# Optimization experiments

Measured on AMD Instinct MI355X. Metric: run time of the kernel, lower is better.

## Reference

```python
import jax, jax.numpy as jnp
import numpy as np

PAD = 32      # person_attrs_dim
NZ = 64       # num_zones
T = 32768     # number of timesteps
D = PAD + 1 + NZ  # 97, input dim to the MLP


def _ln(x, g, b, eps=1e-5):
    # LayerNorm over the last (only) axis of a 1-D vector
    m = jnp.mean(x)
    v = jnp.mean((x - m) ** 2)
    return g * (x - m) / jnp.sqrt(v + eps) + b


def setup_inputs() -> dict:
    key = jax.random.key(0)
    ks = jax.random.split(key, 24)

    def xav(k, shape):  # xavier_normal_ for nn.Linear weight [out, in]
        std = np.sqrt(2.0 / (shape[0] + shape[1])).astype(np.float32)
        return std * jax.random.normal(k, shape, dtype=jnp.float32)

    def lng(k, n):  # layernorm gain (perturbed from 1 so grads are non-trivial)
        return 1.0 + 0.1 * jax.random.normal(k, (n,), dtype=jnp.float32)

    def lnb(k, n):
        return 0.1 * jax.random.normal(k, (n,), dtype=jnp.float32)

    inp = {
        "person_attrs": jax.random.normal(ks[0], (PAD,), dtype=jnp.float32),
        "times": jax.random.uniform(ks[1], (T,), dtype=jnp.float32) * 24.0,
        "zone_features": jax.random.normal(ks[2], (NZ, 16), dtype=jnp.float32),
        "edge_index": jax.random.randint(ks[3], (2, 256), 0, NZ, dtype=jnp.int32),
        # input_norm
        "g0": lng(ks[4], D), "b0": lnb(ks[5], D),
        # encoder1: Linear(D,256) + LN(256)
        "W1": xav(ks[6], (256, D)), "b1": jnp.zeros((256,), jnp.float32),
        "g1": lng(ks[7], 256), "be1": lnb(ks[8], 256),
        # encoder2: Linear(256,128) + LN(128)
        "W2": xav(ks[9], (128, 256)), "b2": jnp.zeros((128,), jnp.float32),
        "g2": lng(ks[10], 128), "be2": lnb(ks[11], 128),
        # output_layer: Linear(128,64) + LN(64) + Linear(64,NZ)
        "W3": xav(ks[12], (64, 128)), "b3": jnp.zeros((64,), jnp.float32),
        "g3": lng(ks[13], 64), "be3": lnb(ks[14], 64),
        "W4": xav(ks[15], (NZ, 64)), "b4": jnp.zeros((NZ,), jnp.float32),
    }
    return inp


def reference(person_attrs, times, zone_features, edge_index,
              g0, b0, W1, b1, g1, be1, W2, b2, g2, be2,
              W3, b3, g3, be3, W4, b4):
    nz = W4.shape[0]
    # set_graph_data: symmetric adjacency with self-loops (zone_features unused)
    u, v = edge_index[0], edge_index[1]
    A = jnp.zeros((nz, nz), jnp.float32).at[u, v].set(1.0).at[v, u].set(1.0)
    A = jnp.maximum(A, jnp.eye(nz, dtype=jnp.float32))

    def step(zone, t):
        onehot = jax.nn.one_hot(zone, nz, dtype=jnp.float32)
        x = jnp.concatenate([person_attrs, t[None], onehot])  # [D]
        x = _ln(x, g0, b0)
        h = jax.nn.relu(_ln(W1 @ x + b1, g1, be1))   # dropout is eval-mode identity
        h = jax.nn.relu(_ln(W2 @ h + b2, g2, be2))
        h = jax.nn.relu(_ln(W3 @ h + b3, g3, be3))
        raw = W4 @ h + b4                            # [nz] raw logits
        row = A[zone]
        # (raw/temp with invalid=-50/temp) * temp  ==  where(valid, raw, -50)
        pred = jnp.where(row > 0, raw, jnp.float32(-50.0))
        nxt = jnp.argmax(jnp.where(row > 0, raw, -jnp.inf)).astype(zone.dtype)
        return nxt, pred

    _, zone_logits = jax.lax.scan(step, jnp.array(0, jnp.int32), times)
    return zone_logits  # [T, nz]
```

## Files before the change

kernel.cpp:

```cpp
#include <hip/hip_runtime.h>
#include <stdint.h>

typedef __attribute__((ext_vector_type(8))) short bf16x8;
typedef __attribute__((ext_vector_type(4))) float f32x4;
typedef __attribute__((ext_vector_type(4))) unsigned int u32x4;
typedef __attribute__((ext_vector_type(2))) unsigned int u32x2;

#define MFMA(a, b, c) __builtin_amdgcn_mfma_f32_16x16x32_bf16(a, b, c, 0, 0, 0)

__device__ __forceinline__ unsigned short f2b(float x) {
  unsigned u = __float_as_uint(x);
  return (unsigned short)((u + 0x7fffu + ((u >> 16) & 1u)) >> 16);
}
__device__ __forceinline__ float b2f(unsigned short h) {
  return __uint_as_float(((unsigned)h) << 16);
}

struct u2 { unsigned hi, lo; };
__device__ __forceinline__ u2 split2(float h0, float h1) {
  unsigned u0 = __float_as_uint(h0), u1 = __float_as_uint(h1);
  u2 r;
  r.hi = (u0 >> 16) | (u1 & 0xffff0000u);
  float r0 = h0 - __uint_as_float(u0 & 0xffff0000u);
  float r1 = h1 - __uint_as_float(u1 & 0xffff0000u);
  r.lo = (__float_as_uint(r0) >> 16) | (__float_as_uint(r1) & 0xffff0000u);
  return r;
}

#define SWZ(row, col) ((col) ^ ((((row) >> 2) & 1) << 4) ^ ((((row) >> 3) & 1) << 2))


__global__ void k_prep(const float* __restrict__ pa, const float* __restrict__ g0,
                       const float* __restrict__ b0, const float* __restrict__ W1,
                       const float* __restrict__ b1,
                       float* __restrict__ c_pa, float* __restrict__ w_t,
                       float* __restrict__ c_g, float* __restrict__ c_const,
                       float* __restrict__ scal, float* __restrict__ wzT,
                       float* __restrict__ wzZ) {
  int j = threadIdx.x;
  const float* wr = W1 + j * 97;
  float cg = 0.f, cc = 0.f, cp = 0.f;
  for (int k = 0; k < 97; ++k) { float w = wr[k]; cg += w * g0[k]; cc += w * b0[k]; }
  for (int k = 0; k < 32; ++k) cp += wr[k] * g0[k] * pa[k];
  c_g[j] = cg;
  c_const[j] = cc + b1[j];
  c_pa[j] = cp;
  w_t[j] = wr[32] * g0[32];
  for (int z = 0; z < 64; ++z) {
    float v = wr[33 + z] * g0[33 + z];
    wzT[j * 64 + z] = v;
    wzZ[z * 256 + j] = v;
  }
  if (j == 0) {
    float s = 0.f, q = 0.f;
    for (int k = 0; k < 32; ++k) { float x = pa[k]; s += x; q += x * x; }
    scal[0] = s; scal[1] = q;
  }
}

__global__ void k_prep2(const float* __restrict__ c_pa, const float* __restrict__ w_t,
                        const float* __restrict__ c_g, const float* __restrict__ c_const,
                        const float* __restrict__ wzT, float* __restrict__ st) {
  int tid = threadIdx.x;
  if (tid < 64) {
    int z = tid;
    float A = 0.f, Q = 0.f, dpa = 0.f, dwt = 0.f, dcg = 0.f, dcc = 0.f;
    for (int k = 0; k < 256; ++k) {
      float wz = wzT[k * 64 + z];
      A += wz; Q = fmaf(wz, wz, Q);
      dpa = fmaf(c_pa[k], wz, dpa);
      dwt = fmaf(w_t[k], wz, dwt);
      dcg = fmaf(c_g[k], wz, dcg);
      dcc = fmaf(c_const[k], wz, dcc);
    }
    st[z] = A; st[64 + z] = Q; st[128 + z] = dpa;
    st[192 + z] = dwt; st[256 + z] = dcg; st[320 + z] = dcc;
  } else {
    int lane = tid - 64;
    float acc[14];
    #pragma unroll
    for (int m = 0; m < 14; ++m) acc[m] = 0.f;
    for (int k = lane; k < 256; k += 64) {
      float P = c_pa[k], W = w_t[k], G = c_g[k], C = c_const[k];
      acc[0] += P; acc[1] += W; acc[2] += G; acc[3] += C;
      acc[4] = fmaf(P, P, acc[4]); acc[5] = fmaf(P, W, acc[5]);
      acc[6] = fmaf(P, G, acc[6]); acc[7] = fmaf(P, C, acc[7]);
      acc[8] = fmaf(W, W, acc[8]); acc[9] = fmaf(W, G, acc[9]);
      acc[10] = fmaf(W, C, acc[10]); acc[11] = fmaf(G, G, acc[11]);
      acc[12] = fmaf(G, C, acc[12]); acc[13] = fmaf(C, C, acc[13]);
    }
    #pragma unroll
    for (int off = 1; off < 64; off <<= 1) {
      #pragma unroll
      for (int m = 0; m < 14; ++m) acc[m] += __shfl_xor(acc[m], off, 64);
    }
    if (lane == 0) {
      #pragma unroll
      for (int m = 0; m < 14; ++m) st[386 + m] = acc[m];
    }
  }
}

__global__ void k_scal2st(const float* __restrict__ scal, float* __restrict__ st) {
  if (threadIdx.x < 2) st[384 + threadIdx.x] = scal[threadIdx.x];
}

__global__ void k_adj(const int* __restrict__ ei, unsigned long long* __restrict__ adj) {
  int t = threadIdx.x;
  if (t < 64) adj[t] = 1ull << t;
  __syncthreads();
  int u = ei[t] & 63, v = ei[256 + t] & 63;
  atomicOr(&adj[u], 1ull << v);
  atomicOr(&adj[v], 1ull << u);
}

__global__ void k_wsplit(const float* __restrict__ W2, const float* __restrict__ W3,
                         const float* __restrict__ W4,
                         unsigned short* __restrict__ W2Ah, unsigned short* __restrict__ W2Al,
                         unsigned short* __restrict__ W3Ah, unsigned short* __restrict__ W3Al,
                         unsigned short* __restrict__ W4Ah, unsigned short* __restrict__ W4Al) {
  int idx = blockIdx.x * 256 + threadIdx.x;
  float w; unsigned short* ph; unsigned short* pl; int o;
  if (idx < 32768) {
    int mt = idx >> 12, kt = (idx >> 9) & 7, lane = (idx >> 3) & 63, j = idx & 7;
    int m = mt * 16 + (lane & 15), k = kt * 32 + (lane >> 4) * 8 + j;
    w = W2[m * 256 + k]; ph = W2Ah; pl = W2Al; o = idx;
  } else if (idx < 40960) {
    int r = idx - 32768;
    int mt = r >> 11, kt = (r >> 9) & 3, lane = (r >> 3) & 63, j = r & 7;
    int m = mt * 16 + (lane & 15), k = kt * 32 + (lane >> 4) * 8 + j;
    w = W3[m * 128 + k]; ph = W3Ah; pl = W3Al; o = r;
  } else if (idx < 45056) {
    int r = idx - 40960;
    int mt = r >> 10, kt = (r >> 9) & 1, lane = (r >> 3) & 63, j = r & 7;
    int m = mt * 16 + (lane & 15), k = kt * 32 + (lane >> 4) * 8 + j;
    w = W4[m * 64 + k]; ph = W4Ah; pl = W4Al; o = r;
  } else return;
  unsigned short hb = f2b(w);
  ph[o] = hb;
  pl[o] = f2b(w - b2f(hb));
}


__global__ __launch_bounds__(256, 4) void k_pass1(
    const float* __restrict__ times,
    const float* __restrict__ c_pa, const float* __restrict__ w_t,
    const float* __restrict__ c_g, const float* __restrict__ c_const,
    const float* __restrict__ wzT, const float* __restrict__ st,
    const unsigned short* __restrict__ W2Ah, const unsigned short* __restrict__ W2Al,
    const unsigned short* __restrict__ W3Ah, const unsigned short* __restrict__ W3Al,
    const unsigned short* __restrict__ W4Ah, const unsigned short* __restrict__ W4Al,
    const float* __restrict__ b2, const float* __restrict__ b3,
    const float* __restrict__ b4,
    const float* __restrict__ g1, const float* __restrict__ be1,
    const float* __restrict__ g2, const float* __restrict__ be2,
    const float* __restrict__ g3, const float* __restrict__ be3,
    const unsigned long long* __restrict__ adj,
    unsigned char* __restrict__ nxt) {
  __shared__ __align__(16) char region[32768];
  __shared__ float u_lds[256];
  __shared__ float ps[512];

  unsigned short* B1hi = (unsigned short*)region;
  unsigned short* B1lo = (unsigned short*)(region + 16384);
  unsigned short* B2hi = (unsigned short*)region;
  unsigned short* B2lo = (unsigned short*)(region + 16384);
  unsigned short* B3hi = (unsigned short*)region;
  unsigned short* B3lo = (unsigned short*)(region + 8192);
  unsigned long long* pk = (unsigned long long*)ps;

  const int tid = threadIdx.x;
  const int lane = tid & 63;
  const int l15 = lane & 15;
  const int lhi = lane >> 4;
  const int w = __builtin_amdgcn_readfirstlane(tid >> 6);
  const int i = blockIdx.x;

  const float t = times[i];
  const float m0 = (st[384] + t + 1.0f) * (1.0f / 97.0f);
  const float e2 = (st[385] + t * t + 1.0f) * (1.0f / 97.0f);
  const float alpha = 1.0f / sqrtf(e2 - m0 * m0 + 1e-5f);
  const float gma = -m0 * alpha;

  const f32x4 zero4 = {0.f, 0.f, 0.f, 0.f};

  {
    int k = tid;
    float u = fmaf(t, w_t[k], c_pa[k]);
    u = fmaf(alpha, u, c_const[k]);
    u = fmaf(gma, c_g[k], u);
    u_lds[k] = u;
    float su = u, sq = u * u;
    #pragma unroll
    for (int off = 1; off < 64; off <<= 1) {
      su += __shfl_xor(su, off, 64);
      sq += __shfl_xor(sq, off, 64);
    }
    if (lane == 0) { ps[w] = su; ps[256 + w] = sq; }
  }
  __syncthreads();
  float mu1, inv1;
  {
    float U1 = ps[0] + ps[1] + ps[2] + ps[3];
    float Qu = ps[256] + ps[257] + ps[258] + ps[259];
    float A1 = st[lane], Qz = st[64 + lane];
    float dpa = st[128 + lane], dwt = st[192 + lane];
    float dcg = st[256 + lane], dcc = st[320 + lane];
    float s1 = fmaf(alpha, A1, U1);
    float uwz = fmaf(alpha, fmaf(t, dwt, dpa), fmaf(gma, dcg, dcc));
    float s2 = Qu + 2.0f * alpha * uwz + alpha * alpha * Qz;
    mu1 = s1 * (1.0f / 256.0f);
    inv1 = 1.0f / sqrtf(s2 * (1.0f / 256.0f) - mu1 * mu1 + 1e-5f);
  }

  f32x4 acc[2][4];
  #pragma unroll
  for (int a = 0; a < 2; ++a)
    #pragma unroll
    for (int b = 0; b < 4; ++b) acc[a][b] = zero4;

  u32x4 hh[4], hl[4];

  #pragma unroll
  for (int q = 0; q < 4; ++q) {
    int kb = w * 32 + q * 8;
    f32x4 u0 = *(const f32x4*)(u_lds + kb);
    f32x4 u1v = *(const f32x4*)(u_lds + kb + 4);
    float hbuf[8];
    #pragma unroll
    for (int j = 0; j < 8; ++j) {
      int k = kb + j;
      float u = (j < 4) ? u0[j] : u1v[j - 4];
      float p = fmaf(alpha, wzT[k * 64 + lane], u);
      float gi = g1[k] * inv1;
      float bb = fmaf(-mu1, gi, be1[k]);
      hbuf[j] = fmaxf(fmaf(p, gi, bb), 0.f);
    }
    #pragma unroll
    for (int e = 0; e < 4; ++e) {
      u2 s = split2(hbuf[2 * e], hbuf[2 * e + 1]);
      hh[q][e] = s.hi; hl[q][e] = s.lo;
    }
  }
  #pragma unroll
  for (int q = 0; q < 4; ++q) {
    int slotd = ((w * 4 + lhi) * 64 + q * 16 + l15) * 4;
    *(u32x4*)((unsigned*)B1hi + slotd) = hh[q];
    *(u32x4*)((unsigned*)B1lo + slotd) = hl[q];
  }
  __syncthreads();

  #pragma unroll
  for (int q = 0; q < 4; ++q) {
    int kb = 128 + w * 32 + q * 8;
    f32x4 u0 = *(const f32x4*)(u_lds + kb);
    f32x4 u1v = *(const f32x4*)(u_lds + kb + 4);
    float hbuf[8];
    #pragma unroll
    for (int j = 0; j < 8; ++j) {
      int k = kb + j;
      float u = (j < 4) ? u0[j] : u1v[j - 4];
      float p = fmaf(alpha, wzT[k * 64 + lane], u);
      float gi = g1[k] * inv1;
      float bb = fmaf(-mu1, gi, be1[k]);
      hbuf[j] = fmaxf(fmaf(p, gi, bb), 0.f);
    }
    #pragma unroll
    for (int e = 0; e < 4; ++e) {
      u2 s = split2(hbuf[2 * e], hbuf[2 * e + 1]);
      hh[q][e] = s.hi; hl[q][e] = s.lo;
    }
  }
  for (int kt = 0; kt < 4; ++kt) {
    bf16x8 a0h = *(const bf16x8*)(W2Ah + (((2 * w + 0) * 8 + kt) * 64 + lane) * 8);
    bf16x8 a0l = *(const bf16x8*)(W2Al + (((2 * w + 0) * 8 + kt) * 64 + lane) * 8);
    bf16x8 a1h = *(const bf16x8*)(W2Ah + (((2 * w + 1) * 8 + kt) * 64 + lane) * 8);
    bf16x8 a1l = *(const bf16x8*)(W2Al + (((2 * w + 1) * 8 + kt) * 64 + lane) * 8);
    #pragma unroll
    for (int nt = 0; nt < 4; ++nt) {
      bf16x8 bh = *(const bf16x8*)(B1hi + ((kt * 4 + nt) * 64 + lane) * 8);
      bf16x8 bl = *(const bf16x8*)(B1lo + ((kt * 4 + nt) * 64 + lane) * 8);
      acc[0][nt] = MFMA(a0h, bh, acc[0][nt]);
      acc[0][nt] = MFMA(a0h, bl, acc[0][nt]);
      acc[0][nt] = MFMA(a0l, bh, acc[0][nt]);
      acc[1][nt] = MFMA(a1h, bh, acc[1][nt]);
      acc[1][nt] = MFMA(a1h, bl, acc[1][nt]);
      acc[1][nt] = MFMA(a1l, bh, acc[1][nt]);
    }
  }
  __syncthreads();
  #pragma unroll
  for (int q = 0; q < 4; ++q) {
    int slotd = ((w * 4 + lhi) * 64 + q * 16 + l15) * 4;
    *(u32x4*)((unsigned*)B1hi + slotd) = hh[q];
    *(u32x4*)((unsigned*)B1lo + slotd) = hl[q];
  }
  __syncthreads();
  for (int kt = 0; kt < 4; ++kt) {
    int ktg = 4 + kt;
    bf16x8 a0h = *(const bf16x8*)(W2Ah + (((2 * w + 0) * 8 + ktg) * 64 + lane) * 8);
    bf16x8 a0l = *(const bf16x8*)(W2Al + (((2 * w + 0) * 8 + ktg) * 64 + lane) * 8);
    bf16x8 a1h = *(const bf16x8*)(W2Ah + (((2 * w + 1) * 8 + ktg) * 64 + lane) * 8);
    bf16x8 a1l = *(const bf16x8*)(W2Al + (((2 * w + 1) * 8 + ktg) * 64 + lane) * 8);
    #pragma unroll
    for (int nt = 0; nt < 4; ++nt) {
      bf16x8 bh = *(const bf16x8*)(B1hi + ((kt * 4 + nt) * 64 + lane) * 8);
      bf16x8 bl = *(const bf16x8*)(B1lo + ((kt * 4 + nt) * 64 + lane) * 8);
      acc[0][nt] = MFMA(a0h, bh, acc[0][nt]);
      acc[0][nt] = MFMA(a0h, bl, acc[0][nt]);
      acc[0][nt] = MFMA(a0l, bh, acc[0][nt]);
      acc[1][nt] = MFMA(a1h, bh, acc[1][nt]);
      acc[1][nt] = MFMA(a1h, bl, acc[1][nt]);
      acc[1][nt] = MFMA(a1l, bh, acc[1][nt]);
    }
  }

  #pragma unroll
  for (int mti = 0; mti < 2; ++mti) {
    f32x4 bv = *(const f32x4*)(b2 + w * 32 + mti * 16 + lhi * 4);
    #pragma unroll
    for (int nt = 0; nt < 4; ++nt) acc[mti][nt] += bv;
  }
  {
    #pragma unroll
    for (int nt = 0; nt < 4; ++nt) {
      float x1 = 0.f, x2 = 0.f;
      #pragma unroll
      for (int mti = 0; mti < 2; ++mti)
        #pragma unroll
        for (int r = 0; r < 4; ++r) { float v = acc[mti][nt][r]; x1 += v; x2 += v * v; }
      x1 += __shfl_xor(x1, 16, 64); x1 += __shfl_xor(x1, 32, 64);
      x2 += __shfl_xor(x2, 16, 64); x2 += __shfl_xor(x2, 32, 64);
      if (lane < 16) {
        ps[w * 64 + nt * 16 + lane] = x1;
        ps[256 + w * 64 + nt * 16 + lane] = x2;
      }
    }
  }
  __syncthreads();

  {
    float mu2v[4], iv2v[4];
    #pragma unroll
    for (int nt = 0; nt < 4; ++nt) {
      int c = nt * 16 + l15;
      float a = ps[c] + ps[64 + c] + ps[128 + c] + ps[192 + c];
      float b = ps[256 + c] + ps[320 + c] + ps[384 + c] + ps[448 + c];
      mu2v[nt] = a * (1.0f / 128.0f);
      iv2v[nt] = 1.0f / sqrtf(b * (1.0f / 128.0f) - mu2v[nt] * mu2v[nt] + 1e-5f);
    }
    f32x4 g2v[2], be2v[2];
    #pragma unroll
    for (int mti = 0; mti < 2; ++mti) {
      g2v[mti]  = *(const f32x4*)(g2  + w * 32 + mti * 16 + lhi * 4);
      be2v[mti] = *(const f32x4*)(be2 + w * 32 + mti * 16 + lhi * 4);
    }
    #pragma unroll
    for (int mti = 0; mti < 2; ++mti)
      #pragma unroll
      for (int nt = 0; nt < 4; ++nt) {
        float h[4];
        #pragma unroll
        for (int r = 0; r < 4; ++r) {
          float G = g2v[mti][r] * iv2v[nt];
          float B = fmaf(-mu2v[nt], G, be2v[mti][r]);
          h[r] = fmaxf(fmaf(acc[mti][nt][r], G, B), 0.f);
        }
        u2 s01 = split2(h[0], h[1]);
        u2 s23 = split2(h[2], h[3]);
        int base = ((w * 4 + nt) * 64 + (2 * mti + (lhi >> 1)) * 16 + l15) * 8
                 + 4 * (lhi & 1);
        u32x2 vh = {s01.hi, s23.hi};
        u32x2 vl = {s01.lo, s23.lo};
        *(u32x2*)(B2hi + base) = vh;
        *(u32x2*)(B2lo + base) = vl;
      }
  }
  __syncthreads();

  f32x4 acc2[4];
  #pragma unroll
  for (int b = 0; b < 4; ++b) acc2[b] = zero4;
  for (int kt = 0; kt < 4; ++kt) {
    bf16x8 ah = *(const bf16x8*)(W3Ah + ((w * 4 + kt) * 64 + lane) * 8);
    bf16x8 al = *(const bf16x8*)(W3Al + ((w * 4 + kt) * 64 + lane) * 8);
    #pragma unroll
    for (int nt = 0; nt < 4; ++nt) {
      bf16x8 bh = *(const bf16x8*)(B2hi + ((kt * 4 + nt) * 64 + lane) * 8);
      bf16x8 bl = *(const bf16x8*)(B2lo + ((kt * 4 + nt) * 64 + lane) * 8);
      acc2[nt] = MFMA(ah, bh, acc2[nt]);
      acc2[nt] = MFMA(ah, bl, acc2[nt]);
      acc2[nt] = MFMA(al, bh, acc2[nt]);
    }
  }
  {
    f32x4 bv = *(const f32x4*)(b3 + w * 16 + lhi * 4);
    #pragma unroll
    for (int nt = 0; nt < 4; ++nt) acc2[nt] += bv;
  }
  {
    #pragma unroll
    for (int nt = 0; nt < 4; ++nt) {
      float x1 = 0.f, x2 = 0.f;
      #pragma unroll
      for (int r = 0; r < 4; ++r) { float v = acc2[nt][r]; x1 += v; x2 += v * v; }
      x1 += __shfl_xor(x1, 16, 64); x1 += __shfl_xor(x1, 32, 64);
      x2 += __shfl_xor(x2, 16, 64); x2 += __shfl_xor(x2, 32, 64);
      if (lane < 16) {
        ps[w * 64 + nt * 16 + lane] = x1;
        ps[256 + w * 64 + nt * 16 + lane] = x2;
      }
    }
  }
  __syncthreads();

  {
    float mu3v[4], iv3v[4];
    #pragma unroll
    for (int nt = 0; nt < 4; ++nt) {
      int c = nt * 16 + l15;
      float a = ps[c] + ps[64 + c] + ps[128 + c] + ps[192 + c];
      float b = ps[256 + c] + ps[320 + c] + ps[384 + c] + ps[448 + c];
      mu3v[nt] = a * (1.0f / 64.0f);
      iv3v[nt] = 1.0f / sqrtf(b * (1.0f / 64.0f) - mu3v[nt] * mu3v[nt] + 1e-5f);
    }
    f32x4 g3v  = *(const f32x4*)(g3  + w * 16 + lhi * 4);
    f32x4 be3v = *(const f32x4*)(be3 + w * 16 + lhi * 4);
    #pragma unroll
    for (int nt = 0; nt < 4; ++nt) {
      float h[4];
      #pragma unroll
      for (int r = 0; r < 4; ++r) {
        float G = g3v[r] * iv3v[nt];
        float B = fmaf(-mu3v[nt], G, be3v[r]);
        h[r] = fmaxf(fmaf(acc2[nt][r], G, B), 0.f);
      }
      u2 s01 = split2(h[0], h[1]);
      u2 s23 = split2(h[2], h[3]);
      int base = (((w >> 1) * 4 + nt) * 64 + (2 * (w & 1) + (lhi >> 1)) * 16 + l15) * 8
               + 4 * (lhi & 1);
      u32x2 vh = {s01.hi, s23.hi};
      u32x2 vl = {s01.lo, s23.lo};
      *(u32x2*)(B3hi + base) = vh;
      *(u32x2*)(B3lo + base) = vl;
    }
  }
  __syncthreads();

  f32x4 acc3[4];
  #pragma unroll
  for (int b = 0; b < 4; ++b) acc3[b] = zero4;
  for (int kt = 0; kt < 2; ++kt) {
    bf16x8 ah = *(const bf16x8*)(W4Ah + ((w * 2 + kt) * 64 + lane) * 8);
    bf16x8 al = *(const bf16x8*)(W4Al + ((w * 2 + kt) * 64 + lane) * 8);
    #pragma unroll
    for (int nt = 0; nt < 4; ++nt) {
      bf16x8 bh = *(const bf16x8*)(B3hi + ((kt * 4 + nt) * 64 + lane) * 8);
      bf16x8 bl = *(const bf16x8*)(B3lo + ((kt * 4 + nt) * 64 + lane) * 8);
      acc3[nt] = MFMA(ah, bh, acc3[nt]);
      acc3[nt] = MFMA(ah, bl, acc3[nt]);
      acc3[nt] = MFMA(al, bh, acc3[nt]);
    }
  }
  f32x4 b4v = *(const f32x4*)(b4 + w * 16 + lhi * 4);
  unsigned long long kbest[4];
  #pragma unroll
  for (int nt = 0; nt < 4; ++nt) {
    unsigned long long am = adj[nt * 16 + l15];
    unsigned long long kb = 0ull;
    #pragma unroll
    for (int r = 0; r < 4; ++r) {
      int o = w * 16 + lhi * 4 + r;
      float raw = acc3[nt][r] + b4v[r];
      float val = ((am >> o) & 1ull) ? raw : -__builtin_huge_valf();
      unsigned u = __float_as_uint(val);
      u = (u & 0x80000000u) ? ~u : (u | 0x80000000u);
      unsigned long long key = ((unsigned long long)u << 6) | (unsigned long long)(63 - o);
      if (key > kb) kb = key;
    }
    unsigned long long oth = __shfl_xor(kb, 16, 64); if (oth > kb) kb = oth;
    oth = __shfl_xor(kb, 32, 64); if (oth > kb) kb = oth;
    kbest[nt] = kb;
  }
  if (lane < 16) {
    #pragma unroll
    for (int nt = 0; nt < 4; ++nt) pk[w * 64 + nt * 16 + lane] = kbest[nt];
  }
  __syncthreads();
  if (tid < 64) {
    unsigned long long k0 = pk[tid], k1 = pk[64 + tid];
    unsigned long long k2 = pk[128 + tid], k3 = pk[192 + tid];
    unsigned long long a = k0 > k1 ? k0 : k1;
    unsigned long long b = k2 > k3 ? k2 : k3;
    unsigned long long bb = a > b ? a : b;
    nxt[(size_t)i * 64 + tid] = (unsigned char)(63u - (unsigned)(bb & 63ull));
  }
}


__global__ void k_scan_a(const unsigned char* __restrict__ nxt,
                         unsigned char* __restrict__ cmap) {
  int c = blockIdx.x, lane = threadIdx.x;
  int g = lane;
  const unsigned char* p = nxt + (size_t)c * 128 * 64;
  for (int s = 0; s < 128; ++s) {
    int sig = p[s * 64 + lane];
    g = __shfl(sig, g, 64);
  }
  cmap[c * 64 + lane] = (unsigned char)g;
}

__global__ void k_scan_b(const unsigned char* __restrict__ cmap,
                         int* __restrict__ startz) {
  int lane = threadIdx.x;
  int cur = 0;
  for (int c = 0; c < 256; ++c) {
    if (lane == 0) startz[c] = cur;
    int row = cmap[c * 64 + lane];
    cur = __shfl(row, cur, 64);
  }
}

__global__ void k_scan_c(const unsigned char* __restrict__ nxt,
                         const int* __restrict__ startz,
                         unsigned char* __restrict__ zones) {
  int c = blockIdx.x, lane = threadIdx.x;
  int cur = startz[c];
  const unsigned char* p = nxt + (size_t)c * 128 * 64;
  for (int s = 0; s < 128; ++s) {
    if (lane == 0) zones[c * 128 + s] = (unsigned char)cur;
    int row = p[s * 64 + lane];
    cur = __shfl(row, cur, 64);
  }
}


__global__ __launch_bounds__(256, 2) void k_pass2m(
    const float* __restrict__ times, const unsigned char* __restrict__ zones,
    const float* __restrict__ c_pa, const float* __restrict__ w_t,
    const float* __restrict__ c_g, const float* __restrict__ c_const,
    const float* __restrict__ wzZ, const float* __restrict__ st,
    const unsigned short* __restrict__ W2Ah, const unsigned short* __restrict__ W2Al,
    const unsigned short* __restrict__ W3Ah, const unsigned short* __restrict__ W3Al,
    const unsigned short* __restrict__ W4Ah, const unsigned short* __restrict__ W4Al,
    const float* __restrict__ b2, const float* __restrict__ b3,
    const float* __restrict__ b4,
    const float* __restrict__ g1, const float* __restrict__ be1,
    const float* __restrict__ g2, const float* __restrict__ be2,
    const float* __restrict__ g3, const float* __restrict__ be3,
    const unsigned long long* __restrict__ adj,
    float* __restrict__ out) {
  __shared__ __align__(16) char region[32768];
  __shared__ float ps1[256], ps2[256];
  __shared__ unsigned long long am_lds[64];

  unsigned short* B1hi = (unsigned short*)region;
  unsigned short* B1lo = (unsigned short*)(region + 16384);
  float* h2p = (float*)region;
  unsigned short* B2hi = (unsigned short*)region;
  unsigned short* B2lo = (unsigned short*)(region + 16384);
  float* h3p = (float*)region;
  unsigned short* B3hi = (unsigned short*)(region + 16384);
  unsigned short* B3lo = (unsigned short*)(region + 24576);
  float* outT = (float*)region;

  const int tid = threadIdx.x;
  const int lane = tid & 63;
  const int l15 = lane & 15;
  const int lhi = lane >> 4;
  const int w = __builtin_amdgcn_readfirstlane(tid >> 6);
  const int i0 = blockIdx.x * 64;

  const float t = times[i0 + lane];
  const int z = zones[i0 + lane];
  const int zrow = z << 8;
  if (tid < 64) am_lds[tid] = adj[zones[i0 + tid]];

  const float m0 = (st[384] + t + 1.0f) * (1.0f / 97.0f);
  const float e2 = (st[385] + t * t + 1.0f) * (1.0f / 97.0f);
  const float a0 = 1.0f / sqrtf(e2 - m0 * m0 + 1e-5f);
  const float a1 = a0 * t;
  const float a2 = -m0 * a0;

  float mu1, inv1;
  {
    float SP = st[386], SW = st[387], SG = st[388], SC = st[389];
    float PP = st[390], PW = st[391], PG = st[392], PC = st[393];
    float WW = st[394], WG = st[395], WC = st[396];
    float GG = st[397], GC = st[398], CC = st[399];
    float U1 = a0 * SP + a1 * SW + a2 * SG + SC;
    float s1 = fmaf(a0, st[z], U1);
    float Qu = a0 * a0 * PP + a1 * a1 * WW + a2 * a2 * GG + CC
             + 2.0f * (a0 * a1 * PW + a0 * a2 * PG + a0 * PC
                       + a1 * a2 * WG + a1 * WC + a2 * GC);
    float uwz = a0 * st[128 + z] + a1 * st[192 + z] + a2 * st[256 + z] + st[320 + z];
    float s2 = Qu + 2.0f * a0 * uwz + a0 * a0 * st[64 + z];
    mu1 = s1 * (1.0f / 256.0f);
    inv1 = 1.0f / sqrtf(s2 * (1.0f / 256.0f) - mu1 * mu1 + 1e-5f);
  }

  const f32x4 zero4 = {0.f, 0.f, 0.f, 0.f};
  f32x4 acc[2][4];
  #pragma unroll
  for (int a = 0; a < 2; ++a)
    #pragma unroll
    for (int b = 0; b < 4; ++b) acc[a][b] = zero4;

  for (int kc = 0; kc < 2; ++kc) {
    if (kc) __syncthreads();
    #pragma unroll
    for (int q = 0; q < 4; ++q) {
      int kb = kc * 128 + w * 32 + q * 8;
      float hbuf[8];
      #pragma unroll
      for (int j = 0; j < 8; ++j) {
        int k = kb + j;
        float u = fmaf(a0, c_pa[k], fmaf(a1, w_t[k], fmaf(a2, c_g[k], c_const[k])));
        float p = fmaf(a0, wzZ[zrow + k], u);
        float gi = g1[k] * inv1;
        float bb = fmaf(-mu1, gi, be1[k]);
        hbuf[j] = fmaxf(fmaf(p, gi, bb), 0.f);
      }
      u32x4 vh, vl;
      #pragma unroll
      for (int e = 0; e < 4; ++e) {
        u2 s = split2(hbuf[2 * e], hbuf[2 * e + 1]);
        vh[e] = s.hi; vl[e] = s.lo;
      }
      int slotd = ((w * 4 + lhi) * 64 + q * 16 + l15) * 4;
      *(u32x4*)((unsigned*)B1hi + slotd) = vh;
      *(u32x4*)((unsigned*)B1lo + slotd) = vl;
    }
    __syncthreads();
    for (int kt = 0; kt < 4; ++kt) {
      int ktg = kc * 4 + kt;
      bf16x8 a0h = *(const bf16x8*)(W2Ah + (((2 * w + 0) * 8 + ktg) * 64 + lane) * 8);
      bf16x8 a0l = *(const bf16x8*)(W2Al + (((2 * w + 0) * 8 + ktg) * 64 + lane) * 8);
      bf16x8 a1h = *(const bf16x8*)(W2Ah + (((2 * w + 1) * 8 + ktg) * 64 + lane) * 8);
      bf16x8 a1l = *(const bf16x8*)(W2Al + (((2 * w + 1) * 8 + ktg) * 64 + lane) * 8);
      #pragma unroll
      for (int nt = 0; nt < 4; ++nt) {
        bf16x8 bh = *(const bf16x8*)(B1hi + ((kt * 4 + nt) * 64 + lane) * 8);
        bf16x8 bl = *(const bf16x8*)(B1lo + ((kt * 4 + nt) * 64 + lane) * 8);
        acc[0][nt] = MFMA(a0h, bh, acc[0][nt]);
        acc[0][nt] = MFMA(a0h, bl, acc[0][nt]);
        acc[0][nt] = MFMA(a0l, bh, acc[0][nt]);
        acc[1][nt] = MFMA(a1h, bh, acc[1][nt]);
        acc[1][nt] = MFMA(a1h, bl, acc[1][nt]);
        acc[1][nt] = MFMA(a1l, bh, acc[1][nt]);
      }
    }
  }
  #pragma unroll
  for (int mti = 0; mti < 2; ++mti) {
    f32x4 bv = *(const f32x4*)(b2 + w * 32 + mti * 16 + lhi * 4);
    #pragma unroll
    for (int nt = 0; nt < 4; ++nt) acc[mti][nt] += bv;
  }
  {
    float sa[4], sb[4];
    #pragma unroll
    for (int nt = 0; nt < 4; ++nt) {
      float x1 = 0.f, x2 = 0.f;
      #pragma unroll
      for (int mti = 0; mti < 2; ++mti)
        #pragma unroll
        for (int r = 0; r < 4; ++r) { float v = acc[mti][nt][r]; x1 += v; x2 += v * v; }
      x1 += __shfl_xor(x1, 16, 64); x1 += __shfl_xor(x1, 32, 64);
      x2 += __shfl_xor(x2, 16, 64); x2 += __shfl_xor(x2, 32, 64);
      sa[nt] = x1; sb[nt] = x2;
    }
    if (lane < 16) {
      #pragma unroll
      for (int nt = 0; nt < 4; ++nt) {
        ps1[w * 64 + nt * 16 + lane] = sa[nt];
        ps2[w * 64 + nt * 16 + lane] = sb[nt];
      }
    }
  }
  __syncthreads();
  #pragma unroll
  for (int mti = 0; mti < 2; ++mti)
    #pragma unroll
    for (int nt = 0; nt < 4; ++nt)
      #pragma unroll
      for (int r = 0; r < 4; ++r) {
        int row = w * 32 + mti * 16 + lhi * 4 + r;
        h2p[row * 64 + SWZ(row, nt * 16 + l15)] = acc[mti][nt][r];
      }
  __syncthreads();

  float mu2, inv2;
  {
    float a = ps1[lane] + ps1[64 + lane] + ps1[128 + lane] + ps1[192 + lane];
    float b = ps2[lane] + ps2[64 + lane] + ps2[128 + lane] + ps2[192 + lane];
    mu2 = a * (1.0f / 128.0f);
    inv2 = 1.0f / sqrtf(b * (1.0f / 128.0f) - mu2 * mu2 + 1e-5f);
  }
  float hv[32];
  #pragma unroll
  for (int mi = 0; mi < 32; ++mi) {
    int row = w * 32 + mi;
    hv[mi] = h2p[row * 64 + SWZ(row, lane)];
  }
  __syncthreads();
  #pragma unroll
  for (int q = 0; q < 4; ++q) {
    float hbuf[8];
    #pragma unroll
    for (int j = 0; j < 8; ++j) {
      int mi = q * 8 + j, mm = w * 32 + mi;
      float gi = g2[mm] * inv2;
      float bb = fmaf(-mu2, gi, be2[mm]);
      hbuf[j] = fmaxf(fmaf(hv[mi], gi, bb), 0.f);
    }
    u32x4 vh, vl;
    #pragma unroll
    for (int e = 0; e < 4; ++e) {
      u2 s = split2(hbuf[2 * e], hbuf[2 * e + 1]);
      vh[e] = s.hi; vl[e] = s.lo;
    }
    int slotd = ((w * 4 + lhi) * 64 + q * 16 + l15) * 4;
    *(u32x4*)((unsigned*)B2hi + slotd) = vh;
    *(u32x4*)((unsigned*)B2lo + slotd) = vl;
  }
  __syncthreads();

  f32x4 acc2[4];
  #pragma unroll
  for (int b = 0; b < 4; ++b) acc2[b] = zero4;
  for (int kt = 0; kt < 4; ++kt) {
    bf16x8 ah = *(const bf16x8*)(W3Ah + ((w * 4 + kt) * 64 + lane) * 8);
    bf16x8 al = *(const bf16x8*)(W3Al + ((w * 4 + kt) * 64 + lane) * 8);
    #pragma unroll
    for (int nt = 0; nt < 4; ++nt) {
      bf16x8 bh = *(const bf16x8*)(B2hi + ((kt * 4 + nt) * 64 + lane) * 8);
      bf16x8 bl = *(const bf16x8*)(B2lo + ((kt * 4 + nt) * 64 + lane) * 8);
      acc2[nt] = MFMA(ah, bh, acc2[nt]);
      acc2[nt] = MFMA(ah, bl, acc2[nt]);
      acc2[nt] = MFMA(al, bh, acc2[nt]);
    }
  }
  {
    f32x4 bv = *(const f32x4*)(b3 + w * 16 + lhi * 4);
    #pragma unroll
    for (int nt = 0; nt < 4; ++nt) acc2[nt] += bv;
  }
  {
    float sa[4], sb[4];
    #pragma unroll
    for (int nt = 0; nt < 4; ++nt) {
      float x1 = 0.f, x2 = 0.f;
      #pragma unroll
      for (int r = 0; r < 4; ++r) { float v = acc2[nt][r]; x1 += v; x2 += v * v; }
      x1 += __shfl_xor(x1, 16, 64); x1 += __shfl_xor(x1, 32, 64);
      x2 += __shfl_xor(x2, 16, 64); x2 += __shfl_xor(x2, 32, 64);
      sa[nt] = x1; sb[nt] = x2;
    }
    if (lane < 16) {
      #pragma unroll
      for (int nt = 0; nt < 4; ++nt) {
        ps1[w * 64 + nt * 16 + lane] = sa[nt];
        ps2[w * 64 + nt * 16 + lane] = sb[nt];
      }
    }
  }
  __syncthreads();
  #pragma unroll
  for (int nt = 0; nt < 4; ++nt)
    #pragma unroll
    for (int r = 0; r < 4; ++r) {
      int row = w * 16 + lhi * 4 + r;
      h3p[row * 64 + SWZ(row, nt * 16 + l15)] = acc2[nt][r];
    }
  __syncthreads();

  float mu3, inv3;
  {
    float a = ps1[lane] + ps1[64 + lane] + ps1[128 + lane] + ps1[192 + lane];
    float b = ps2[lane] + ps2[64 + lane] + ps2[128 + lane] + ps2[192 + lane];
    mu3 = a * (1.0f / 64.0f);
    inv3 = 1.0f / sqrtf(b * (1.0f / 64.0f) - mu3 * mu3 + 1e-5f);
  }
  #pragma unroll
  for (int q = 0; q < 2; ++q) {
    int o = w * 2 + q;
    float hbuf[8];
    #pragma unroll
    for (int j = 0; j < 8; ++j) {
      int mm = o * 8 + j;
      float v = h3p[mm * 64 + SWZ(mm, lane)];
      float gi = g3[mm] * inv3;
      float bb = fmaf(-mu3, gi, be3[mm]);
      hbuf[j] = fmaxf(fmaf(v, gi, bb), 0.f);
    }
    u32x4 vh, vl;
    #pragma unroll
    for (int e = 0; e < 4; ++e) {
      u2 s = split2(hbuf[2 * e], hbuf[2 * e + 1]);
      vh[e] = s.hi; vl[e] = s.lo;
    }
    int slotd = (((o >> 2) * 4 + lhi) * 64 + (o & 3) * 16 + l15) * 4;
    *(u32x4*)((unsigned*)B3hi + slotd) = vh;
    *(u32x4*)((unsigned*)B3lo + slotd) = vl;
  }
  __syncthreads();

  f32x4 acc3[4];
  #pragma unroll
  for (int b = 0; b < 4; ++b) acc3[b] = zero4;
  for (int kt = 0; kt < 2; ++kt) {
    bf16x8 ah = *(const bf16x8*)(W4Ah + ((w * 2 + kt) * 64 + lane) * 8);
    bf16x8 al = *(const bf16x8*)(W4Al + ((w * 2 + kt) * 64 + lane) * 8);
    #pragma unroll
    for (int nt = 0; nt < 4; ++nt) {
      bf16x8 bh = *(const bf16x8*)(B3hi + ((kt * 4 + nt) * 64 + lane) * 8);
      bf16x8 bl = *(const bf16x8*)(B3lo + ((kt * 4 + nt) * 64 + lane) * 8);
      acc3[nt] = MFMA(ah, bh, acc3[nt]);
      acc3[nt] = MFMA(ah, bl, acc3[nt]);
      acc3[nt] = MFMA(al, bh, acc3[nt]);
    }
  }
  f32x4 b4v = *(const f32x4*)(b4 + w * 16 + lhi * 4);
  #pragma unroll
  for (int nt = 0; nt < 4; ++nt) {
    unsigned long long am = am_lds[nt * 16 + l15];
    #pragma unroll
    for (int r = 0; r < 4; ++r) {
      int o = w * 16 + lhi * 4 + r;
      float raw = acc3[nt][r] + b4v[r];
      float predv = ((am >> o) & 1ull) ? raw : -50.0f;
      int b = nt * 16 + l15;
      outT[b * 64 + SWZ(b, o)] = predv;
    }
  }
  __syncthreads();
  {
    int b = tid >> 2, cb = (tid & 3) * 16;
    size_t gbase = ((size_t)(i0 + b)) * 64 + cb;
    #pragma unroll
    for (int c4 = 0; c4 < 4; ++c4) {
      int col = cb + c4 * 4;
      f32x4 v = *(const f32x4*)(outT + b * 64 + SWZ(b, col));
      *(f32x4*)(out + gbase + c4 * 4) = v;
    }
  }
}


extern "C" void kernel_launch(void* const* d_in, const int* in_sizes, int n_in,
                              void* d_out, int out_size, void* d_ws, size_t ws_size,
                              hipStream_t stream) {
  const float* pa    = (const float*)d_in[0];
  const float* times = (const float*)d_in[1];
  const int*   ei    = (const int*)d_in[3];
  const float* g0    = (const float*)d_in[4];
  const float* b0    = (const float*)d_in[5];
  const float* W1    = (const float*)d_in[6];
  const float* b1    = (const float*)d_in[7];
  const float* g1    = (const float*)d_in[8];
  const float* be1   = (const float*)d_in[9];
  const float* W2    = (const float*)d_in[10];
  const float* b2    = (const float*)d_in[11];
  const float* g2    = (const float*)d_in[12];
  const float* be2   = (const float*)d_in[13];
  const float* W3    = (const float*)d_in[14];
  const float* b3    = (const float*)d_in[15];
  const float* g3    = (const float*)d_in[16];
  const float* be3   = (const float*)d_in[17];
  const float* W4    = (const float*)d_in[18];
  const float* b4    = (const float*)d_in[19];

  char* ws = (char*)d_ws;
  float* c_pa    = (float*)(ws + 0);
  float* w_t     = (float*)(ws + 1024);
  float* c_g     = (float*)(ws + 2048);
  float* c_const = (float*)(ws + 3072);
  float* scal    = (float*)(ws + 4096);
  unsigned long long* adj = (unsigned long long*)(ws + 4608);
  float* wzT = (float*)(ws + 5120);
  float* wzZ = (float*)(ws + 70656);
  unsigned short* W2Ah = (unsigned short*)(ws + 136192);
  unsigned short* W2Al = (unsigned short*)(ws + 201728);
  unsigned short* W3Ah = (unsigned short*)(ws + 267264);
  unsigned short* W3Al = (unsigned short*)(ws + 283648);
  unsigned short* W4Ah = (unsigned short*)(ws + 300032);
  unsigned short* W4Al = (unsigned short*)(ws + 308224);
  float* st = (float*)(ws + 316416);
  unsigned char* nxt  = (unsigned char*)(ws + 318464);
  unsigned char* cmap = (unsigned char*)(ws + 2415616);
  int* startz = (int*)(ws + 2432000);
  unsigned char* zones = (unsigned char*)(ws + 2433024);

  k_prep<<<1, 256, 0, stream>>>(pa, g0, b0, W1, b1, c_pa, w_t, c_g, c_const,
                                scal, wzT, wzZ);
  k_prep2<<<1, 128, 0, stream>>>(c_pa, w_t, c_g, c_const, wzT, st);
  k_scal2st<<<1, 64, 0, stream>>>(scal, st);
  k_adj<<<1, 256, 0, stream>>>(ei, adj);
  k_wsplit<<<176, 256, 0, stream>>>(W2, W3, W4, W2Ah, W2Al, W3Ah, W3Al, W4Ah, W4Al);
  k_pass1<<<32768, 256, 0, stream>>>(times, c_pa, w_t, c_g, c_const, wzT, st,
                                     W2Ah, W2Al, W3Ah, W3Al, W4Ah, W4Al,
                                     b2, b3, b4, g1, be1, g2, be2, g3, be3,
                                     adj, nxt);
  k_scan_a<<<256, 64, 0, stream>>>(nxt, cmap);
  k_scan_b<<<1, 64, 0, stream>>>(cmap, startz);
  k_scan_c<<<256, 64, 0, stream>>>(nxt, startz, zones);
  k_pass2m<<<512, 256, 0, stream>>>(times, zones, c_pa, w_t, c_g, c_const,
                                    wzZ, st, W2Ah, W2Al, W3Ah, W3Al, W4Ah, W4Al,
                                    b2, b3, b4, g1, be1, g2, be2, g3, be3,
                                    adj, (float*)d_out);
}
```

Measured before the change: 833.7 us.

## Halve LDS staging buffer with K-chunked layer loops to double occupancy

The shared staging region drops from 32 KB to 16 KB. Layer-2 and layer-3 matmuls now run in smaller K chunks, each with its own fill/sync/consume phase, and launch bounds go from 4 to 8 blocks per SM so more blocks can be resident. LayerNorm statistics for layers 2 and 3 are now reduced once by wave 0 and broadcast through LDS, instead of every wave recomputing them. The trade-off is more __syncthreads barriers per block, and some waves sit idle during the chunked layer-3 input writes.

```diff
diff --git a/kernel.cpp b/kernel.cpp
--- a/kernel.cpp
+++ b/kernel.cpp
@@ -142,7 +142,7 @@
 }
 
 
-__global__ __launch_bounds__(256, 4) void k_pass1(
+__global__ __launch_bounds__(256, 8) void k_pass1(
     const float* __restrict__ times,
     const float* __restrict__ c_pa, const float* __restrict__ w_t,
     const float* __restrict__ c_g, const float* __restrict__ c_const,
@@ -157,16 +157,12 @@
     const float* __restrict__ g3, const float* __restrict__ be3,
     const unsigned long long* __restrict__ adj,
     unsigned char* __restrict__ nxt) {
-  __shared__ __align__(16) char region[32768];
+  __shared__ __align__(16) char region[16384];
   __shared__ float u_lds[256];
   __shared__ float ps[512];
 
-  unsigned short* B1hi = (unsigned short*)region;
-  unsigned short* B1lo = (unsigned short*)(region + 16384);
-  unsigned short* B2hi = (unsigned short*)region;
-  unsigned short* B2lo = (unsigned short*)(region + 16384);
-  unsigned short* B3hi = (unsigned short*)region;
-  unsigned short* B3lo = (unsigned short*)(region + 8192);
+  unsigned short* Bhi = (unsigned short*)region;
+  unsigned short* Blo = (unsigned short*)(region + 8192);
   unsigned long long* pk = (unsigned long long*)ps;
 
   const int tid = threadIdx.x;
@@ -219,99 +215,53 @@
     #pragma unroll
     for (int b = 0; b < 4; ++b) acc[a][b] = zero4;
 
-  u32x4 hh[4], hl[4];
-
-  #pragma unroll
-  for (int q = 0; q < 4; ++q) {
-    int kb = w * 32 + q * 8;
-    f32x4 u0 = *(const f32x4*)(u_lds + kb);
-    f32x4 u1v = *(const f32x4*)(u_lds + kb + 4);
-    float hbuf[8];
-    #pragma unroll
-    for (int j = 0; j < 8; ++j) {
-      int k = kb + j;
-      float u = (j < 4) ? u0[j] : u1v[j - 4];
-      float p = fmaf(alpha, wzT[k * 64 + lane], u);
-      float gi = g1[k] * inv1;
-      float bb = fmaf(-mu1, gi, be1[k]);
-      hbuf[j] = fmaxf(fmaf(p, gi, bb), 0.f);
-    }
-    #pragma unroll
-    for (int e = 0; e < 4; ++e) {
-      u2 s = split2(hbuf[2 * e], hbuf[2 * e + 1]);
-      hh[q][e] = s.hi; hl[q][e] = s.lo;
-    }
-  }
-  #pragma unroll
-  for (int q = 0; q < 4; ++q) {
-    int slotd = ((w * 4 + lhi) * 64 + q * 16 + l15) * 4;
-    *(u32x4*)((unsigned*)B1hi + slotd) = hh[q];
-    *(u32x4*)((unsigned*)B1lo + slotd) = hl[q];
-  }
-  __syncthreads();
-
-  #pragma unroll
-  for (int q = 0; q < 4; ++q) {
-    int kb = 128 + w * 32 + q * 8;
-    f32x4 u0 = *(const f32x4*)(u_lds + kb);
-    f32x4 u1v = *(const f32x4*)(u_lds + kb + 4);
-    float hbuf[8];
-    #pragma unroll
-    for (int j = 0; j < 8; ++j) {
-      int k = kb + j;
-      float u = (j < 4) ? u0[j] : u1v[j - 4];
-      float p = fmaf(alpha, wzT[k * 64 + lane], u);
-      float gi = g1[k] * inv1;
-      float bb = fmaf(-mu1, gi, be1[k]);
-      hbuf[j] = fmaxf(fmaf(p, gi, bb), 0.f);
-    }
-    #pragma unroll
-    for (int e = 0; e < 4; ++e) {
-      u2 s = split2(hbuf[2 * e], hbuf[2 * e + 1]);
-      hh[q][e] = s.hi; hl[q][e] = s.lo;
-    }
-  }
-  for (int kt = 0; kt < 4; ++kt) {
-    bf16x8 a0h = *(const bf16x8*)(W2Ah + (((2 * w + 0) * 8 + kt) * 64 + lane) * 8);
-    bf16x8 a0l = *(const bf16x8*)(W2Al + (((2 * w + 0) * 8 + kt) * 64 + lane) * 8);
-    bf16x8 a1h = *(const bf16x8*)(W2Ah + (((2 * w + 1) * 8 + kt) * 64 + lane) * 8);
-    bf16x8 a1l = *(const bf16x8*)(W2Al + (((2 * w + 1) * 8 + kt) * 64 + lane) * 8);
-    #pragma unroll
-    for (int nt = 0; nt < 4; ++nt) {
-      bf16x8 bh = *(const bf16x8*)(B1hi + ((kt * 4 + nt) * 64 + lane) * 8);
-      bf16x8 bl = *(const bf16x8*)(B1lo + ((kt * 4 + nt) * 64 + lane) * 8);
-      acc[0][nt] = MFMA(a0h, bh, acc[0][nt]);
-      acc[0][nt] = MFMA(a0h, bl, acc[0][nt]);
-      acc[0][nt] = MFMA(a0l, bh, acc[0][nt]);
-      acc[1][nt] = MFMA(a1h, bh, acc[1][nt]);
-      acc[1][nt] = MFMA(a1h, bl, acc[1][nt]);
-      acc[1][nt] = MFMA(a1l, bh, acc[1][nt]);
-    }
-  }
-  __syncthreads();
-  #pragma unroll
-  for (int q = 0; q < 4; ++q) {
-    int slotd = ((w * 4 + lhi) * 64 + q * 16 + l15) * 4;
-    *(u32x4*)((unsigned*)B1hi + slotd) = hh[q];
-    *(u32x4*)((unsigned*)B1lo + slotd) = hl[q];
-  }
-  __syncthreads();
-  for (int kt = 0; kt < 4; ++kt) {
-    int ktg = 4 + kt;
-    bf16x8 a0h = *(const bf16x8*)(W2Ah + (((2 * w + 0) * 8 + ktg) * 64 + lane) * 8);
-    bf16x8 a0l = *(const bf16x8*)(W2Al + (((2 * w + 0) * 8 + ktg) * 64 + lane) * 8);
-    bf16x8 a1h = *(const bf16x8*)(W2Ah + (((2 * w + 1) * 8 + ktg) * 64 + lane) * 8);
-    bf16x8 a1l = *(const bf16x8*)(W2Al + (((2 * w + 1) * 8 + ktg) * 64 + lane) * 8);
-    #pragma unroll
-    for (int nt = 0; nt < 4; ++nt) {
-      bf16x8 bh = *(const bf16x8*)(B1hi + ((kt * 4 + nt) * 64 + lane) * 8);
-      bf16x8 bl = *(const bf16x8*)(B1lo + ((kt * 4 + nt) * 64 + lane) * 8);
-      acc[0][nt] = MFMA(a0h, bh, acc[0][nt]);
-      acc[0][nt] = MFMA(a0h, bl, acc[0][nt]);
-      acc[0][nt] = MFMA(a0l, bh, acc[0][nt]);
-      acc[1][nt] = MFMA(a1h, bh, acc[1][nt]);
-      acc[1][nt] = MFMA(a1h, bl, acc[1][nt]);
-      acc[1][nt] = MFMA(a1l, bh, acc[1][nt]);
+  for (int kc = 0; kc < 4; ++kc) {
+    if (kc) __syncthreads();
+    #pragma unroll
+    for (int q = 0; q < 2; ++q) {
+      int o = w * 2 + q;
+      int kb = kc * 64 + o * 8;
+      f32x4 u0 = *(const f32x4*)(u_lds + kb);
+      f32x4 u1v = *(const f32x4*)(u_lds + kb + 4);
+      float hbuf[8];
+      #pragma unroll
+      for (int j = 0; j < 8; ++j) {
+        int k = kb + j;
+        float u = (j < 4) ? u0[j] : u1v[j - 4];
+        float p = fmaf(alpha, wzT[k * 64 + lane], u);
+        float gi = g1[k] * inv1;
+        float bb = fmaf(-mu1, gi, be1[k]);
+        hbuf[j] = fmaxf(fmaf(p, gi, bb), 0.f);
+      }
+      u32x4 vh, vl;
+      #pragma unroll
+      for (int e = 0; e < 4; ++e) {
+        u2 s = split2(hbuf[2 * e], hbuf[2 * e + 1]);
+        vh[e] = s.hi; vl[e] = s.lo;
+      }
+      int slotd = (((o >> 2) * 4 + lhi) * 64 + (o & 3) * 16 + l15) * 4;
+      *(u32x4*)((unsigned*)Bhi + slotd) = vh;
+      *(u32x4*)((unsigned*)Blo + slotd) = vl;
+    }
+    __syncthreads();
+    #pragma unroll
+    for (int kt = 0; kt < 2; ++kt) {
+      int ktg = kc * 2 + kt;
+      bf16x8 a0h = *(const bf16x8*)(W2Ah + (((2 * w + 0) * 8 + ktg) * 64 + lane) * 8);
+      bf16x8 a0l = *(const bf16x8*)(W2Al + (((2 * w + 0) * 8 + ktg) * 64 + lane) * 8);
+      bf16x8 a1h = *(const bf16x8*)(W2Ah + (((2 * w + 1) * 8 + ktg) * 64 + lane) * 8);
+      bf16x8 a1l = *(const bf16x8*)(W2Al + (((2 * w + 1) * 8 + ktg) * 64 + lane) * 8);
+      #pragma unroll
+      for (int nt = 0; nt < 4; ++nt) {
+        bf16x8 bh = *(const bf16x8*)(Bhi + ((kt * 4 + nt) * 64 + lane) * 8);
+        bf16x8 bl = *(const bf16x8*)(Blo + ((kt * 4 + nt) * 64 + lane) * 8);
+        acc[0][nt] = MFMA(a0h, bh, acc[0][nt]);
+        acc[0][nt] = MFMA(a0h, bl, acc[0][nt]);
+        acc[0][nt] = MFMA(a0l, bh, acc[0][nt]);
+        acc[1][nt] = MFMA(a1h, bh, acc[1][nt]);
+        acc[1][nt] = MFMA(a1h, bl, acc[1][nt]);
+        acc[1][nt] = MFMA(a1l, bh, acc[1][nt]);
+      }
     }
   }
 
@@ -321,128 +271,135 @@
     #pragma unroll
     for (int nt = 0; nt < 4; ++nt) acc[mti][nt] += bv;
   }
-  {
-    #pragma unroll
-    for (int nt = 0; nt < 4; ++nt) {
-      float x1 = 0.f, x2 = 0.f;
-      #pragma unroll
-      for (int mti = 0; mti < 2; ++mti)
+  #pragma unroll
+  for (int nt = 0; nt < 4; ++nt) {
+    float x1 = 0.f, x2 = 0.f;
+    #pragma unroll
+    for (int mti = 0; mti < 2; ++mti)
+      #pragma unroll
+      for (int r = 0; r < 4; ++r) { float v = acc[mti][nt][r]; x1 += v; x2 += v * v; }
+    x1 += __shfl_xor(x1, 16, 64); x1 += __shfl_xor(x1, 32, 64);
+    x2 += __shfl_xor(x2, 16, 64); x2 += __shfl_xor(x2, 32, 64);
+    if (lane < 16) {
+      ps[w * 64 + nt * 16 + lane] = x1;
+      ps[256 + w * 64 + nt * 16 + lane] = x2;
+    }
+  }
+  __syncthreads();
+  if (w == 0) {
+    int c = lane;
+    float a = ps[c] + ps[64 + c] + ps[128 + c] + ps[192 + c];
+    float b = ps[256 + c] + ps[320 + c] + ps[384 + c] + ps[448 + c];
+    float mu = a * (1.0f / 128.0f);
+    float inv = 1.0f / sqrtf(b * (1.0f / 128.0f) - mu * mu + 1e-5f);
+    ps[c] = inv;
+    ps[64 + c] = -mu * inv;
+  }
+  __syncthreads();
+
+  f32x4 acc2[4];
+  #pragma unroll
+  for (int b = 0; b < 4; ++b) acc2[b] = zero4;
+
+  for (int kc2 = 0; kc2 < 2; ++kc2) {
+    if ((w >> 1) == kc2) {
+      f32x4 g2v[2], be2v[2];
+      #pragma unroll
+      for (int mti = 0; mti < 2; ++mti) {
+        g2v[mti]  = *(const f32x4*)(g2  + w * 32 + mti * 16 + lhi * 4);
+        be2v[mti] = *(const f32x4*)(be2 + w * 32 + mti * 16 + lhi * 4);
+      }
+      #pragma unroll
+      for (int nt = 0; nt < 4; ++nt) {
+        int c = nt * 16 + l15;
+        float P = ps[c], Q = ps[64 + c];
         #pragma unroll
-        for (int r = 0; r < 4; ++r) { float v = acc[mti][nt][r]; x1 += v; x2 += v * v; }
-      x1 += __shfl_xor(x1, 16, 64); x1 += __shfl_xor(x1, 32, 64);
-      x2 += __shfl_xor(x2, 16, 64); x2 += __shfl_xor(x2, 32, 64);
-      if (lane < 16) {
-        ps[w * 64 + nt * 16 + lane] = x1;
-        ps[256 + w * 64 + nt * 16 + lane] = x2;
-      }
-    }
-  }
-  __syncthreads();
-
-  {
-    float mu2v[4], iv2v[4];
+        for (int mti = 0; mti < 2; ++mti) {
+          float h[4];
+          #pragma unroll
+          for (int r = 0; r < 4; ++r) {
+            float G = g2v[mti][r];
+            h[r] = fmaxf(fmaf(acc[mti][nt][r], G * P, fmaf(G, Q, be2v[mti][r])), 0.f);
+          }
+          u2 s01 = split2(h[0], h[1]);
+          u2 s23 = split2(h[2], h[3]);
+          int base = (((w - 2 * kc2) * 4 + nt) * 64 +
+                      (mti * 2 + (lhi >> 1)) * 16 + l15) * 8 + (lhi & 1) * 4;
+          u32x2 vh = {s01.hi, s23.hi};
+          u32x2 vl = {s01.lo, s23.lo};
+          *(u32x2*)(Bhi + base) = vh;
+          *(u32x2*)(Blo + base) = vl;
+        }
+      }
+    }
+    __syncthreads();
+    #pragma unroll
+    for (int kt = 0; kt < 2; ++kt) {
+      int ktg = kc2 * 2 + kt;
+      bf16x8 ah = *(const bf16x8*)(W3Ah + ((w * 4 + ktg) * 64 + lane) * 8);
+      bf16x8 al = *(const bf16x8*)(W3Al + ((w * 4 + ktg) * 64 + lane) * 8);
+      #pragma unroll
+      for (int nt = 0; nt < 4; ++nt) {
+        bf16x8 bh = *(const bf16x8*)(Bhi + ((kt * 4 + nt) * 64 + lane) * 8);
+        bf16x8 bl = *(const bf16x8*)(Blo + ((kt * 4 + nt) * 64 + lane) * 8);
+        acc2[nt] = MFMA(ah, bh, acc2[nt]);
+        acc2[nt] = MFMA(ah, bl, acc2[nt]);
+        acc2[nt] = MFMA(al, bh, acc2[nt]);
+      }
+    }
+    __syncthreads();
+  }
+
+  {
+    f32x4 bv = *(const f32x4*)(b3 + w * 16 + lhi * 4);
+    #pragma unroll
+    for (int nt = 0; nt < 4; ++nt) acc2[nt] += bv;
+  }
+  #pragma unroll
+  for (int nt = 0; nt < 4; ++nt) {
+    float x1 = 0.f, x2 = 0.f;
+    #pragma unroll
+    for (int r = 0; r < 4; ++r) { float v = acc2[nt][r]; x1 += v; x2 += v * v; }
+    x1 += __shfl_xor(x1, 16, 64); x1 += __shfl_xor(x1, 32, 64);
+    x2 += __shfl_xor(x2, 16, 64); x2 += __shfl_xor(x2, 32, 64);
+    if (lane < 16) {
+      ps[w * 64 + nt * 16 + lane] = x1;
+      ps[256 + w * 64 + nt * 16 + lane] = x2;
+    }
+  }
+  __syncthreads();
+  if (w == 0) {
+    int c = lane;
+    float a = ps[c] + ps[64 + c] + ps[128 + c] + ps[192 + c];
+    float b = ps[256 + c] + ps[320 + c] + ps[384 + c] + ps[448 + c];
+    float mu = a * (1.0f / 64.0f);
+    float inv = 1.0f / sqrtf(b * (1.0f / 64.0f) - mu * mu + 1e-5f);
+    ps[c] = inv;
+    ps[64 + c] = -mu * inv;
+  }
+  __syncthreads();
+
+  {
+    f32x4 g3v  = *(const f32x4*)(g3  + w * 16 + lhi * 4);
+    f32x4 be3v = *(const f32x4*)(be3 + w * 16 + lhi * 4);
     #pragma unroll
     for (int nt = 0; nt < 4; ++nt) {
       int c = nt * 16 + l15;
-      float a = ps[c] + ps[64 + c] + ps[128 + c] + ps[192 + c];
-      float b = ps[256 + c] + ps[320 + c] + ps[384 + c] + ps[448 + c];
-      mu2v[nt] = a * (1.0f / 128.0f);
-      iv2v[nt] = 1.0f / sqrtf(b * (1.0f / 128.0f) - mu2v[nt] * mu2v[nt] + 1e-5f);
-    }
-    f32x4 g2v[2], be2v[2];
-    #pragma unroll
-    for (int mti = 0; mti < 2; ++mti) {
-      g2v[mti]  = *(const f32x4*)(g2  + w * 32 + mti * 16 + lhi * 4);
-      be2v[mti] = *(const f32x4*)(be2 + w * 32 + mti * 16 + lhi * 4);
-    }
-    #pragma unroll
-    for (int mti = 0; mti < 2; ++mti)
-      #pragma unroll
-      for (int nt = 0; nt < 4; ++nt) {
-        float h[4];
-        #pragma unroll
-        for (int r = 0; r < 4; ++r) {
-          float G = g2v[mti][r] * iv2v[nt];
-          float B = fmaf(-mu2v[nt], G, be2v[mti][r]);
-          h[r] = fmaxf(fmaf(acc[mti][nt][r], G, B), 0.f);
-        }
-        u2 s01 = split2(h[0], h[1]);
-        u2 s23 = split2(h[2], h[3]);
-        int base = ((w * 4 + nt) * 64 + (2 * mti + (lhi >> 1)) * 16 + l15) * 8
-                 + 4 * (lhi & 1);
-        u32x2 vh = {s01.hi, s23.hi};
-        u32x2 vl = {s01.lo, s23.lo};
-        *(u32x2*)(B2hi + base) = vh;
-        *(u32x2*)(B2lo + base) = vl;
-      }
-  }
-  __syncthreads();
-
-  f32x4 acc2[4];
-  #pragma unroll
-  for (int b = 0; b < 4; ++b) acc2[b] = zero4;
-  for (int kt = 0; kt < 4; ++kt) {
-    bf16x8 ah = *(const bf16x8*)(W3Ah + ((w * 4 + kt) * 64 + lane) * 8);
-    bf16x8 al = *(const bf16x8*)(W3Al + ((w * 4 + kt) * 64 + lane) * 8);
-    #pragma unroll
-    for (int nt = 0; nt < 4; ++nt) {
-      bf16x8 bh = *(const bf16x8*)(B2hi + ((kt * 4 + nt) * 64 + lane) * 8);
-      bf16x8 bl = *(const bf16x8*)(B2lo + ((kt * 4 + nt) * 64 + lane) * 8);
-      acc2[nt] = MFMA(ah, bh, acc2[nt]);
-      acc2[nt] = MFMA(ah, bl, acc2[nt]);
-      acc2[nt] = MFMA(al, bh, acc2[nt]);
-    }
-  }
-  {
-    f32x4 bv = *(const f32x4*)(b3 + w * 16 + lhi * 4);
-    #pragma unroll
-    for (int nt = 0; nt < 4; ++nt) acc2[nt] += bv;
-  }
-  {
-    #pragma unroll
-    for (int nt = 0; nt < 4; ++nt) {
-      float x1 = 0.f, x2 = 0.f;
-      #pragma unroll
-      for (int r = 0; r < 4; ++r) { float v = acc2[nt][r]; x1 += v; x2 += v * v; }
-      x1 += __shfl_xor(x1, 16, 64); x1 += __shfl_xor(x1, 32, 64);
-      x2 += __shfl_xor(x2, 16, 64); x2 += __shfl_xor(x2, 32, 64);
-      if (lane < 16) {
-        ps[w * 64 + nt * 16 + lane] = x1;
-        ps[256 + w * 64 + nt * 16 + lane] = x2;
-      }
-    }
-  }
-  __syncthreads();
-
-  {
-    float mu3v[4], iv3v[4];
-    #pragma unroll
-    for (int nt = 0; nt < 4; ++nt) {
-      int c = nt * 16 + l15;
-      float a = ps[c] + ps[64 + c] + ps[128 + c] + ps[192 + c];
-      float b = ps[256 + c] + ps[320 + c] + ps[384 + c] + ps[448 + c];
-      mu3v[nt] = a * (1.0f / 64.0f);
-      iv3v[nt] = 1.0f / sqrtf(b * (1.0f / 64.0f) - mu3v[nt] * mu3v[nt] + 1e-5f);
-    }
-    f32x4 g3v  = *(const f32x4*)(g3  + w * 16 + lhi * 4);
-    f32x4 be3v = *(const f32x4*)(be3 + w * 16 + lhi * 4);
-    #pragma unroll
-    for (int nt = 0; nt < 4; ++nt) {
+      float P = ps[c], Q = ps[64 + c];
       float h[4];
       #pragma unroll
       for (int r = 0; r < 4; ++r) {
-        float G = g3v[r] * iv3v[nt];
-        float B = fmaf(-mu3v[nt], G, be3v[r]);
-        h[r] = fmaxf(fmaf(acc2[nt][r], G, B), 0.f);
+        float G = g3v[r];
+        h[r] = fmaxf(fmaf(acc2[nt][r], G * P, fmaf(G, Q, be3v[r])), 0.f);
       }
       u2 s01 = split2(h[0], h[1]);
       u2 s23 = split2(h[2], h[3]);
-      int base = (((w >> 1) * 4 + nt) * 64 + (2 * (w & 1) + (lhi >> 1)) * 16 + l15) * 8
-               + 4 * (lhi & 1);
+      int base = (((w >> 1) * 4 + nt) * 64 +
+                  ((w & 1) * 2 + (lhi >> 1)) * 16 + l15) * 8 + (lhi & 1) * 4;
       u32x2 vh = {s01.hi, s23.hi};
       u32x2 vl = {s01.lo, s23.lo};
-      *(u32x2*)(B3hi + base) = vh;
-      *(u32x2*)(B3lo + base) = vl;
+      *(u32x2*)(Bhi + base) = vh;
+      *(u32x2*)(Blo + base) = vl;
     }
   }
   __syncthreads();
@@ -450,13 +407,14 @@
   f32x4 acc3[4];
   #pragma unroll
   for (int b = 0; b < 4; ++b) acc3[b] = zero4;
+  #pragma unroll
   for (int kt = 0; kt < 2; ++kt) {
     bf16x8 ah = *(const bf16x8*)(W4Ah + ((w * 2 + kt) * 64 + lane) * 8);
     bf16x8 al = *(const bf16x8*)(W4Al + ((w * 2 + kt) * 64 + lane) * 8);
     #pragma unroll
     for (int nt = 0; nt < 4; ++nt) {
-      bf16x8 bh = *(const bf16x8*)(B3hi + ((kt * 4 + nt) * 64 + lane) * 8);
-      bf16x8 bl = *(const bf16x8*)(B3lo + ((kt * 4 + nt) * 64 + lane) * 8);
+      bf16x8 bh = *(const bf16x8*)(Bhi + ((kt * 4 + nt) * 64 + lane) * 8);
+      bf16x8 bl = *(const bf16x8*)(Blo + ((kt * 4 + nt) * 64 + lane) * 8);
       acc3[nt] = MFMA(ah, bh, acc3[nt]);
       acc3[nt] = MFMA(ah, bl, acc3[nt]);
       acc3[nt] = MFMA(al, bh, acc3[nt]);
```

New measurement: 1.289 ms. +54.6%, slower.
